# Kernel tuning notes

Hardware: AMD Instinct MI355X
Metric: run time of the kernel (lower is better)

The kernel has to match this reference:

```python
import jax, jax.numpy as jnp
import numpy as np

N = 65536      # total voxels (lidar + image tokens)
D = 256        # d_model
H = 8          # nhead
DFF = 2048     # dim_feedforward
SS = 128       # set_size
SN = 512       # set_num (SN * SS == N, each partition is a permutation of all voxels)
NSHIFT = 2


def setup_inputs() -> dict:
    key = jax.random.key(0)
    ks = jax.random.split(key, 10)
    src = jax.random.normal(ks[0], (N, D), jnp.float32)
    pos_embed = jax.random.normal(ks[1], (NSHIFT, N, D), jnp.float32) * 0.02
    # each (shift, set_id) partition covers every voxel exactly once
    inds = jnp.stack([
        jnp.stack([
            jax.random.permutation(jax.random.fold_in(ks[2], s * 2 + p), N).reshape(SN, SS)
            for p in range(2)
        ])
        for s in range(NSHIFT)
    ]).astype(jnp.int32)                      # (NSHIFT, 2, SN, SS)
    masks = jax.random.uniform(ks[3], (NSHIFT, 2, SN, SS)) < 0.1
    masks = masks.at[..., 0].set(False)       # keep at least one key per set
    init = lambda k, shape: jax.random.normal(k, shape, jnp.float32) * 0.02
    return {
        'src': src, 'pos_embed': pos_embed,
        'set_voxel_inds': inds, 'set_voxel_masks': masks,
        'w_qkv': init(ks[4], (2, 3 * D, D)), 'b_qkv': jnp.zeros((2, 3 * D)),
        'w_out': init(ks[5], (2, D, D)), 'b_out': jnp.zeros((2, D)),
        'w_ff1': init(ks[6], (2, DFF, D)), 'b_ff1': jnp.zeros((2, DFF)),
        'w_ff2': init(ks[7], (2, D, DFF)), 'b_ff2': jnp.zeros((2, D)),
        'g_n1': jnp.ones((2, D)), 'b_n1': jnp.zeros((2, D)),
        'g_n2': jnp.ones((2, D)), 'b_n2': jnp.zeros((2, D)),
        'g_ln': jnp.ones((2, D)), 'b_ln': jnp.zeros((2, D)),
    }


def _ln(x, g, b):
    m = jnp.mean(x, -1, keepdims=True)
    v = jnp.mean(jnp.square(x - m), -1, keepdims=True)
    return (x - m) * jax.lax.rsqrt(v + 1e-5) * g + b


def _mha(q_in, k_in, v_in, mask, wqkv, bqkv, wo, bo):
    # q_in/k_in/v_in: (SN, SS, D); mask: (SN, SS) True = ignore key
    wq, wk, wv = jnp.split(wqkv, 3, axis=0)
    bq, bk, bv = jnp.split(bqkv, 3, axis=0)
    hd = D // H
    q = (q_in @ wq.T + bq).reshape(SN, SS, H, hd)
    k = (k_in @ wk.T + bk).reshape(SN, SS, H, hd)
    v = (v_in @ wv.T + bv).reshape(SN, SS, H, hd)
    scores = jnp.einsum('bqhd,bkhd->bhqk', q, k) / np.float32(np.sqrt(hd))
    scores = jnp.where(mask[:, None, None, :], jnp.float32(-1e9), scores)
    attn = jax.nn.softmax(scores, axis=-1)
    o = jnp.einsum('bhqk,bkhd->bqhd', attn, v).reshape(SN, SS, D)
    return o @ wo.T + bo


def reference(src, pos_embed, set_voxel_inds, set_voxel_masks,
              w_qkv, b_qkv, w_out, b_out, w_ff1, b_ff1, w_ff2, b_ff2,
              g_n1, b_n1, g_n2, b_n2, g_ln, b_ln):
    out = src
    set_id = 0  # block_id % 2 with block_id == 0
    for i in range(NSHIFT):  # two encoder layers, one per shift
        inds = set_voxel_inds[i, set_id]   # (SN, SS)
        mask = set_voxel_masks[i, set_id]  # (SN, SS)
        pos = pos_embed[i]
        identity = out
        feat = out[inds]                   # gather voxels into sets
        qk = feat + pos[inds]
        a = _mha(qk, qk, feat, mask, w_qkv[i], b_qkv[i], w_out[i], b_out[i])
        # scatter back: per voxel, take its FIRST occurrence in flattened set order
        flat = inds.reshape(-1)
        L = flat.shape[0]
        perm = jnp.full((N,), L, jnp.int32).at[flat].min(jnp.arange(L, dtype=jnp.int32))
        src2 = a.reshape(-1, D)[perm]
        x = _ln(out + src2, g_n1[i], b_n1[i])
        ff = jax.nn.relu(x @ w_ff1[i].T + b_ff1[i]) @ w_ff2[i].T + b_ff2[i]
        x = _ln(x + ff, g_n2[i], b_n2[i])
        out = _ln(x + identity, g_ln[i], b_ln[i])
    return out
```

## Files before the change

kernel.cpp:

```cpp
#include <hip/hip_runtime.h>
#include <math.h>

#define NVOX 65536
#define DM 256
#define NH 8
#define HDIM 32
#define DFFN 2048
#define SSZ 128
#define SNUM 512

#define AS1 __attribute__((address_space(1)))
#define AS3 __attribute__((address_space(3)))

typedef __attribute__((ext_vector_type(8))) __bf16 bf16x8;
typedef __attribute__((ext_vector_type(8))) unsigned short u16x8;
typedef __attribute__((ext_vector_type(4))) float f32x4;

__device__ __forceinline__ unsigned short f2bf(float f) {
    unsigned int u = __float_as_uint(f);
    u += 0x7fffu + ((u >> 16) & 1u);
    return (unsigned short)(u >> 16);
}
__device__ __forceinline__ float bf2f(unsigned short u) {
    return __uint_as_float(((unsigned int)u) << 16);
}

#define VMCNT0 asm volatile("s_waitcnt vmcnt(0)" ::: "memory")
#define VMCNT2 asm volatile("s_waitcnt vmcnt(2)" ::: "memory")
#define VMCNT4 asm volatile("s_waitcnt vmcnt(4)" ::: "memory")
#define LGKM0  asm volatile("s_waitcnt lgkmcnt(0)" ::: "memory")

__global__ __launch_bounds__(256)
void cvt_bf16_kernel(const float* __restrict__ in, unsigned short* __restrict__ out, int n) {
    int i = blockIdx.x * 256 + threadIdx.x;
    int stride = gridDim.x * 256;
    for (; i < n; i += stride) out[i] = f2bf(in[i]);
}

__global__ __launch_bounds__(256)
void gather_kernel(const float* __restrict__ src, const float* __restrict__ pos,
                   const int* __restrict__ inds,
                   unsigned short* __restrict__ qk, unsigned short* __restrict__ feat) {
    int j = blockIdx.x * 4 + (threadIdx.x >> 6);
    int lane = threadIdx.x & 63;
    int v = inds[j];
    float4 a = ((const float4*)(src + (size_t)v * DM))[lane];
    float4 p = ((const float4*)(pos + (size_t)v * DM))[lane];
    ushort4 qo, fo;
    qo.x = f2bf(a.x + p.x); qo.y = f2bf(a.y + p.y);
    qo.z = f2bf(a.z + p.z); qo.w = f2bf(a.w + p.w);
    fo.x = f2bf(a.x); fo.y = f2bf(a.y); fo.z = f2bf(a.z); fo.w = f2bf(a.w);
    ((ushort4*)(qk   + (size_t)j * DM))[lane] = qo;
    ((ushort4*)(feat + (size_t)j * DM))[lane] = fo;
}

template<int EPI, bool RELU>
__global__ __launch_bounds__(512)
void gemm_mfma256(const unsigned short* __restrict__ A, const unsigned short* __restrict__ W,
                  const float* __restrict__ bias, void* __restrict__ Cout,
                  int M, int N, int K,
                  const int* __restrict__ inds,
                  const float* __restrict__ res1,
                  const float* __restrict__ g1, const float* __restrict__ b1,
                  unsigned short* __restrict__ out2) {
    __shared__ alignas(16) char smem[69632];
    unsigned short* As = (unsigned short*)smem;
    unsigned short* Bs = (unsigned short*)(smem + 32768);
    float* ebuf = (float*)smem;
    const int ES = 264;

    int tid = threadIdx.x;
    int wave = tid >> 6, lane = tid & 63;
    int wm = wave >> 2;
    int wn = wave & 3;

    unsigned lin = blockIdx.x + blockIdx.y * gridDim.x;
    unsigned nwg = gridDim.x * gridDim.y;
    unsigned swz = lin;
    if ((nwg & 7u) == 0u) { unsigned cpx = nwg >> 3; swz = (lin & 7u) * cpx + (lin >> 3); }
    int bx = (int)(swz / gridDim.y);
    int by = (int)(swz % gridDim.y);
    int mBase = bx * 256, nBase = by * 256;

    int rr = lane & 15;
    int kq = (lane >> 4) * 8;
    int rbase = (lane >> 4) * 4;

    f32x4 acc[8][4];
    const f32x4 zero = {0.f, 0.f, 0.f, 0.f};
#pragma unroll
    for (int m = 0; m < 8; m++)
#pragma unroll
        for (int n = 0; n < 4; n++) acc[m][n] = zero;

    const unsigned short* gA0 = A + (size_t)(mBase + (wave * 2 + 0) * 16 + rr) * K + kq;
    const unsigned short* gA1 = A + (size_t)(mBase + (wave * 2 + 1) * 16 + rr) * K + kq;
    const unsigned short* gB0 = W + (size_t)(nBase + (wave * 2 + 0) * 16 + rr) * K + kq;
    const unsigned short* gB1 = W + (size_t)(nBase + (wave * 2 + 1) * 16 + rr) * K + kq;

    auto stage = [&](int b, int kt) {
        int ko = kt * 32;
        __builtin_amdgcn_global_load_lds((const AS1 void*)(gA0 + ko),
            (AS3 void*)(As + b * 8192 + (wave * 2 + 0) * 512), 16, 0, 0);
        __builtin_amdgcn_global_load_lds((const AS1 void*)(gA1 + ko),
            (AS3 void*)(As + b * 8192 + (wave * 2 + 1) * 512), 16, 0, 0);
        __builtin_amdgcn_global_load_lds((const AS1 void*)(gB0 + ko),
            (AS3 void*)(Bs + b * 8192 + (wave * 2 + 0) * 512), 16, 0, 0);
        __builtin_amdgcn_global_load_lds((const AS1 void*)(gB1 + ko),
            (AS3 void*)(Bs + b * 8192 + (wave * 2 + 1) * 512), 16, 0, 0);
    };

    int nt = K >> 5;
    stage(0, 0);

    for (int t = 0; t < nt; ++t) {
        int p = t & 1;
        if (t + 1 < nt) { stage(p ^ 1, t + 1); VMCNT4; }
        else { VMCNT0; }
        __builtin_amdgcn_s_barrier();
        __builtin_amdgcn_sched_barrier(0);

        bf16x8 af[8], bf[4];
#pragma unroll
        for (int m = 0; m < 8; m++)
            af[m] = *(const bf16x8*)(As + p * 8192 + (wm * 8 + m) * 512 + lane * 8);
#pragma unroll
        for (int n = 0; n < 4; n++)
            bf[n] = *(const bf16x8*)(Bs + p * 8192 + (wn * 4 + n) * 512 + lane * 8);
#pragma unroll
        for (int m = 0; m < 8; m++)
#pragma unroll
            for (int n = 0; n < 4; n++)
                acc[m][n] = __builtin_amdgcn_mfma_f32_16x16x32_bf16(af[m], bf[n], acc[m][n], 0, 0, 0);

        __builtin_amdgcn_sched_barrier(0);
        __builtin_amdgcn_s_barrier();
    }

    float bn[4];
#pragma unroll
    for (int n = 0; n < 4; n++)
        bn[n] = bias[nBase + wn * 64 + n * 16 + rr];

    int erow = tid >> 3;
    int ec0  = (tid & 7) * 32;
#pragma unroll
    for (int pass = 0; pass < 4; ++pass) {
        __syncthreads();
        if (wm == (pass >> 1)) {
#pragma unroll
            for (int mm = 0; mm < 4; ++mm) {
                int m = (pass & 1) * 4 + mm;
#pragma unroll
                for (int n = 0; n < 4; ++n) {
                    int lcol = wn * 64 + n * 16 + rr;
#pragma unroll
                    for (int r = 0; r < 4; ++r) {
                        float v = acc[m][n][r] + bn[n];
                        if (RELU) v = fmaxf(v, 0.f);
                        ebuf[(mm * 16 + rbase + r) * ES + lcol] = v;
                    }
                }
            }
        }
        __syncthreads();
        int grow = mBase + pass * 64 + erow;

        if constexpr (EPI == 0) {
            unsigned short* dst = (unsigned short*)Cout + (size_t)grow * N + nBase + ec0;
#pragma unroll
            for (int g = 0; g < 4; ++g) {
                u16x8 o;
#pragma unroll
                for (int j = 0; j < 8; ++j)
                    o[j] = f2bf(ebuf[erow * ES + ec0 + g * 8 + j]);
                *(u16x8*)(dst + g * 8) = o;
            }
        } else {
            int v = inds[grow];
            const float* pr = res1 + (size_t)v * 256;
            f32x4 tv[8];
            float s = 0.f, s2 = 0.f;
#pragma unroll
            for (int g = 0; g < 8; ++g) {
                float4 e = *(float4*)(ebuf + erow * ES + ec0 + g * 4);
                float4 p = *(const float4*)(pr + ec0 + g * 4);
                f32x4 t = {e.x + p.x, e.y + p.y, e.z + p.z, e.w + p.w};
                tv[g] = t;
                s += t[0] + t[1] + t[2] + t[3];
                s2 += t[0]*t[0] + t[1]*t[1] + t[2]*t[2] + t[3]*t[3];
            }
#pragma unroll
            for (int off = 1; off < 8; off <<= 1) { s += __shfl_xor(s, off); s2 += __shfl_xor(s2, off); }
            float mean = s * (1.f/256.f);
            float var = fmaf(-mean, mean, s2 * (1.f/256.f));
            float rs = rsqrtf(var + 1e-5f);
            float* xd = (float*)Cout + (size_t)v * 256 + ec0;
            unsigned short* xb = out2 + (size_t)v * 256 + ec0;
#pragma unroll
            for (int g = 0; g < 8; ++g) {
                float4 gg = *(const float4*)(g1 + ec0 + g * 4);
                float4 bb = *(const float4*)(b1 + ec0 + g * 4);
                float4 o;
                o.x = fmaf((tv[g][0] - mean) * rs, gg.x, bb.x);
                o.y = fmaf((tv[g][1] - mean) * rs, gg.y, bb.y);
                o.z = fmaf((tv[g][2] - mean) * rs, gg.z, bb.z);
                o.w = fmaf((tv[g][3] - mean) * rs, gg.w, bb.w);
                *(float4*)(xd + g * 4) = o;
                ushort4 ob; ob.x = f2bf(o.x); ob.y = f2bf(o.y); ob.z = f2bf(o.z); ob.w = f2bf(o.w);
                *(ushort4*)(xb + g * 4) = ob;
            }
        }
    }
}

__global__ __launch_bounds__(512, 2)
void ffn_fused(const unsigned short* __restrict__ X,
               const unsigned short* __restrict__ W1,
               const unsigned short* __restrict__ W2,
               const float* __restrict__ b1g,
               const float* __restrict__ b2g,
               const float* __restrict__ xf,
               const float* __restrict__ prev,
               const float* __restrict__ lnG1, const float* __restrict__ lnB1,
               const float* __restrict__ lnG2, const float* __restrict__ lnB2,
               float* __restrict__ out) {
    __shared__ alignas(16) char smem[163840];
    unsigned short* Xs   = (unsigned short*)smem;
    unsigned short* Wbuf = (unsigned short*)(smem + 65536);
    char*           HsB  = smem + 98304;
    float*          ebuf = (float*)smem;
    const int ES = 264;

    int tid = threadIdx.x;
    int wave = tid >> 6, lane = tid & 63;
    int wm = wave >> 2;
    int wn = wave & 3;
    int mBase = blockIdx.x * 128;
    int rr = lane & 15;
    int kq = (lane >> 4) * 8;
    int rbase = (lane >> 4) * 4;

    auto gll = [&](const unsigned short* g, unsigned short* l) {
        __builtin_amdgcn_global_load_lds((const AS1 void*)g, (AS3 void*)l, 16, 0, 0);
    };

#pragma unroll
    for (int u = 0; u < 8; ++u)
        gll(X + (size_t)(mBase + wave * 16 + rr) * 256 + u * 32 + kq,
            Xs + (wave * 8 + u) * 512);

    auto stage_slice = [&](int s) {
        int c = s >> 4, half = (s >> 3) & 1, kt = s & 7;
        unsigned short* wb = Wbuf + (s & 1) * 8192;
        if (half == 0) {
            gll(W1 + (size_t)(c * 256 + (wave * 2 + 0) * 16 + rr) * 256 + kt * 32 + kq,
                wb + (wave * 2 + 0) * 512);
            gll(W1 + (size_t)(c * 256 + (wave * 2 + 1) * 16 + rr) * 256 + kt * 32 + kq,
                wb + (wave * 2 + 1) * 512);
        } else {
            gll(W2 + (size_t)((wave * 2 + 0) * 16 + rr) * 2048 + c * 256 + kt * 32 + kq,
                wb + (wave * 2 + 0) * 512);
            gll(W2 + (size_t)((wave * 2 + 1) * 16 + rr) * 2048 + c * 256 + kt * 32 + kq,
                wb + (wave * 2 + 1) * 512);
        }
    };

    f32x4 yacc[4][4];
    const f32x4 zero = {0.f, 0.f, 0.f, 0.f};
#pragma unroll
    for (int m = 0; m < 4; m++)
#pragma unroll
        for (int n = 0; n < 4; n++) yacc[m][n] = zero;

    stage_slice(0);
    __syncthreads();

    for (int c = 0; c < 8; ++c) {
        f32x4 hacc[4][4];
#pragma unroll
        for (int m = 0; m < 4; m++)
#pragma unroll
            for (int n = 0; n < 4; n++) hacc[m][n] = zero;

#pragma unroll
        for (int kt = 0; kt < 8; ++kt) {
            int s = c * 16 + kt;
            stage_slice(s + 1);
            VMCNT2;
            __builtin_amdgcn_s_barrier();
            __builtin_amdgcn_sched_barrier(0);

            bf16x8 af[4], bf[4];
#pragma unroll
            for (int m = 0; m < 4; m++)
                af[m] = *(const bf16x8*)(Xs + ((wm * 4 + m) * 8 + kt) * 512 + lane * 8);
#pragma unroll
            for (int n = 0; n < 4; n++)
                bf[n] = *(const bf16x8*)(Wbuf + (s & 1) * 8192 + (wn * 4 + n) * 512 + lane * 8);
#pragma unroll
            for (int m = 0; m < 4; m++)
#pragma unroll
                for (int n = 0; n < 4; n++)
                    hacc[m][n] = __builtin_amdgcn_mfma_f32_16x16x32_bf16(af[m], bf[n], hacc[m][n], 0, 0, 0);

            __builtin_amdgcn_sched_barrier(0);
            __builtin_amdgcn_s_barrier();
        }

        {
            float b1v[4];
#pragma unroll
            for (int n = 0; n < 4; n++)
                b1v[n] = b1g[c * 256 + wn * 64 + n * 16 + rr];
#pragma unroll
            for (int m = 0; m < 4; m++)
#pragma unroll
                for (int n = 0; n < 4; n++)
#pragma unroll
                    for (int r = 0; r < 4; r++) {
                        float v = fmaxf(hacc[m][n][r] + b1v[n], 0.f);
                        int row = wm * 64 + m * 16 + rbase + r;
                        int col = wn * 64 + n * 16 + rr;
                        unsigned byte = (unsigned)(row * 512 + col * 2) ^ ((row & 7) << 4);
                        *(unsigned short*)(HsB + byte) = f2bf(v);
                    }
            LGKM0;
            __builtin_amdgcn_s_barrier();
        }

#pragma unroll
        for (int kt = 0; kt < 8; ++kt) {
            int s = c * 16 + 8 + kt;
            if (s + 1 < 128) { stage_slice(s + 1); VMCNT2; }
            else { VMCNT0; }
            __builtin_amdgcn_s_barrier();
            __builtin_amdgcn_sched_barrier(0);

            bf16x8 af[4], bf[4];
#pragma unroll
            for (int m = 0; m < 4; m++) {
                int row = wm * 64 + m * 16 + rr;
                unsigned byte = (unsigned)(row * 512 + kt * 64 + (lane >> 4) * 16) ^ ((rr & 7) << 4);
                af[m] = *(const bf16x8*)(HsB + byte);
            }
#pragma unroll
            for (int n = 0; n < 4; n++)
                bf[n] = *(const bf16x8*)(Wbuf + (s & 1) * 8192 + (wn * 4 + n) * 512 + lane * 8);
#pragma unroll
            for (int m = 0; m < 4; m++)
#pragma unroll
                for (int n = 0; n < 4; n++)
                    yacc[m][n] = __builtin_amdgcn_mfma_f32_16x16x32_bf16(af[m], bf[n], yacc[m][n], 0, 0, 0);

            __builtin_amdgcn_sched_barrier(0);
            __builtin_amdgcn_s_barrier();
        }
    }

    float b2v[4];
#pragma unroll
    for (int n = 0; n < 4; n++)
        b2v[n] = b2g[wn * 64 + n * 16 + rr];

    int erow = tid >> 5;
    int ec0  = (tid & 31) * 8;
#pragma unroll
    for (int p = 0; p < 8; ++p) {
        __syncthreads();
        if (wm == (p >> 2)) {
            const int m = p & 3;
#pragma unroll
            for (int n = 0; n < 4; ++n) {
                int lcol = wn * 64 + n * 16 + rr;
#pragma unroll
                for (int r = 0; r < 4; ++r)
                    ebuf[(rbase + r) * ES + lcol] = yacc[m][n][r] + b2v[n];
            }
        }
        __syncthreads();
        int grow = mBase + p * 16 + erow;

        float tv[8];
        float s1 = 0.f, s2 = 0.f;
        const float* xr = xf + (size_t)grow * 256 + ec0;
#pragma unroll
        for (int j = 0; j < 8; ++j) {
            float t = ebuf[erow * ES + ec0 + j] + xr[j];
            tv[j] = t; s1 += t; s2 += t * t;
        }
#pragma unroll
        for (int off = 1; off < 32; off <<= 1) { s1 += __shfl_xor(s1, off); s2 += __shfl_xor(s2, off); }
        float mean = s1 * (1.f/256.f);
        float var = fmaf(-mean, mean, s2 * (1.f/256.f));
        float rs = rsqrtf(var + 1e-5f);

        const float* pr = prev + (size_t)grow * 256 + ec0;
        float s3 = 0.f, s4 = 0.f;
#pragma unroll
        for (int j = 0; j < 8; ++j) {
            float u = fmaf((tv[j] - mean) * rs, lnG1[ec0 + j], lnB1[ec0 + j]) + pr[j];
            tv[j] = u; s3 += u; s4 += u * u;
        }
#pragma unroll
        for (int off = 1; off < 32; off <<= 1) { s3 += __shfl_xor(s3, off); s4 += __shfl_xor(s4, off); }
        float mean2 = s3 * (1.f/256.f);
        float var2 = fmaf(-mean2, mean2, s4 * (1.f/256.f));
        float rs2 = rsqrtf(var2 + 1e-5f);

        float* od = out + (size_t)grow * 256 + ec0;
#pragma unroll
        for (int g = 0; g < 2; ++g) {
            float4 o;
            o.x = fmaf((tv[g*4+0] - mean2) * rs2, lnG2[ec0 + g*4+0], lnB2[ec0 + g*4+0]);
            o.y = fmaf((tv[g*4+1] - mean2) * rs2, lnG2[ec0 + g*4+1], lnB2[ec0 + g*4+1]);
            o.z = fmaf((tv[g*4+2] - mean2) * rs2, lnG2[ec0 + g*4+2], lnB2[ec0 + g*4+2]);
            o.w = fmaf((tv[g*4+3] - mean2) * rs2, lnG2[ec0 + g*4+3], lnB2[ec0 + g*4+3]);
            *(float4*)(od + g * 4) = o;
        }
    }
}

__global__ __launch_bounds__(256)
void attn_mfma_kernel(const unsigned short* __restrict__ QK,
                      const unsigned short* __restrict__ V,
                      const unsigned char* __restrict__ mask,
                      unsigned short* __restrict__ ao) {
    int s = blockIdx.x, h = blockIdx.y;
    int tid = threadIdx.x;
    int wq = tid >> 6;
    int lane = tid & 63;

    __shared__ alignas(16) unsigned short Ks[128 * 40];
    __shared__ alignas(16) unsigned short Vt[32 * 136];
    __shared__ alignas(16) unsigned short Plds[4 * 4096];
    __shared__ unsigned char msk[SSZ];

#pragma unroll
    for (int it = 0; it < 2; it++) {
        int idx = tid + it * 256;
        int key = idx >> 2, dimoff = (idx & 3) * 8;
        bf16x8 kv = *(const bf16x8*)(QK + (size_t)(s * SSZ + key) * 512 + 256 + h * HDIM + dimoff);
        *(bf16x8*)(Ks + key * 40 + dimoff) = kv;
        u16x8 vv = *(const u16x8*)(V + (size_t)(s * SSZ + key) * DM + h * HDIM + dimoff);
#pragma unroll
        for (int j = 0; j < 8; j++) Vt[(dimoff + j) * 136 + key] = vv[j];
    }
    if (tid < SSZ) msk[tid] = mask[s * SSZ + tid];
    __syncthreads();

    int rr = lane & 15;
    int kq = (lane >> 4) * 8;
    const f32x4 zero = {0.f, 0.f, 0.f, 0.f};

    bf16x8 qa[2];
#pragma unroll
    for (int mt = 0; mt < 2; mt++)
        qa[mt] = *(const bf16x8*)(QK + (size_t)(s * SSZ + wq * 32 + mt * 16 + rr) * 512 + h * HDIM + kq);

    f32x4 S[2][8];
#pragma unroll
    for (int nt = 0; nt < 8; nt++) {
        bf16x8 kb = *(const bf16x8*)(Ks + (nt * 16 + rr) * 40 + kq);
#pragma unroll
        for (int mt = 0; mt < 2; mt++)
            S[mt][nt] = __builtin_amdgcn_mfma_f32_16x16x32_bf16(qa[mt], kb, zero, 0, 0, 0);
    }

    const float SCALE = 0.17677669529663687f;
    f32x4 rm[2];
#pragma unroll
    for (int mt = 0; mt < 2; mt++) { rm[mt].x = rm[mt].y = rm[mt].z = rm[mt].w = -1e30f; }
#pragma unroll
    for (int nt = 0; nt < 8; nt++) {
        bool mv = msk[nt * 16 + rr] != 0;
#pragma unroll
        for (int mt = 0; mt < 2; mt++) {
#pragma unroll
            for (int r = 0; r < 4; r++) {
                float v = mv ? -1e30f : S[mt][nt][r] * SCALE;
                S[mt][nt][r] = v;
                rm[mt][r] = fmaxf(rm[mt][r], v);
            }
        }
    }
#pragma unroll
    for (int off = 1; off < 16; off <<= 1) {
#pragma unroll
        for (int mt = 0; mt < 2; mt++)
#pragma unroll
            for (int r = 0; r < 4; r++)
                rm[mt][r] = fmaxf(rm[mt][r], __shfl_xor(rm[mt][r], off));
    }

    f32x4 rs[2];
#pragma unroll
    for (int mt = 0; mt < 2; mt++) { rs[mt] = zero; }
#pragma unroll
    for (int nt = 0; nt < 8; nt++)
#pragma unroll
        for (int mt = 0; mt < 2; mt++)
#pragma unroll
            for (int r = 0; r < 4; r++) {
                float p = __expf(S[mt][nt][r] - rm[mt][r]);
                S[mt][nt][r] = p;
                rs[mt][r] += p;
            }
#pragma unroll
    for (int off = 1; off < 16; off <<= 1) {
#pragma unroll
        for (int mt = 0; mt < 2; mt++)
#pragma unroll
            for (int r = 0; r < 4; r++)
                rs[mt][r] += __shfl_xor(rs[mt][r], off);
    }

    char* Pbase = (char*)Plds + wq * 8192;
#pragma unroll
    for (int nt = 0; nt < 8; nt++)
#pragma unroll
        for (int mt = 0; mt < 2; mt++)
#pragma unroll
            for (int r = 0; r < 4; r++) {
                int prow = mt * 16 + (lane >> 4) * 4 + r;
                int col  = nt * 16 + rr;
                unsigned addr = (unsigned)(prow * 256 + col * 2) ^ ((prow & 7) << 4);
                *(unsigned short*)(Pbase + addr) = f2bf(S[mt][nt][r]);
            }
    __syncthreads();

    f32x4 O[2][2];
#pragma unroll
    for (int mt = 0; mt < 2; mt++)
#pragma unroll
        for (int nd = 0; nd < 2; nd++) O[mt][nd] = zero;
#pragma unroll
    for (int kc = 0; kc < 4; kc++) {
        bf16x8 pa[2];
#pragma unroll
        for (int mt = 0; mt < 2; mt++) {
            int prow = mt * 16 + rr;
            unsigned addr = (unsigned)(prow * 256 + (kc * 32 + kq) * 2) ^ ((prow & 7) << 4);
            pa[mt] = *(const bf16x8*)(Pbase + addr);
        }
#pragma unroll
        for (int nd = 0; nd < 2; nd++) {
            bf16x8 vb = *(const bf16x8*)(Vt + (nd * 16 + rr) * 136 + kc * 32 + kq);
#pragma unroll
            for (int mt = 0; mt < 2; mt++)
                O[mt][nd] = __builtin_amdgcn_mfma_f32_16x16x32_bf16(pa[mt], vb, O[mt][nd], 0, 0, 0);
        }
    }

#pragma unroll
    for (int mt = 0; mt < 2; mt++) {
#pragma unroll
        for (int nd = 0; nd < 2; nd++) {
#pragma unroll
            for (int r = 0; r < 4; r++) {
                int row = s * SSZ + wq * 32 + mt * 16 + (lane >> 4) * 4 + r;
                int col = h * HDIM + nd * 16 + rr;
                ao[(size_t)row * DM + col] = f2bf(O[mt][nd][r] / rs[mt][r]);
            }
        }
    }
}

extern "C" void kernel_launch(void* const* d_in, const int* in_sizes, int n_in,
                              void* d_out, int out_size, void* d_ws, size_t ws_size,
                              hipStream_t stream) {
    const float* src       = (const float*)d_in[0];
    const float* pos_embed = (const float*)d_in[1];
    const int*   inds_all  = (const int*)d_in[2];
    const unsigned char* masks_all = (const unsigned char*)d_in[3];
    const float* w_qkv = (const float*)d_in[4];
    const float* b_qkv = (const float*)d_in[5];
    const float* w_out = (const float*)d_in[6];
    const float* b_out = (const float*)d_in[7];
    const float* w_ff1 = (const float*)d_in[8];
    const float* b_ff1 = (const float*)d_in[9];
    const float* w_ff2 = (const float*)d_in[10];
    const float* b_ff2 = (const float*)d_in[11];
    const float* g_n1 = (const float*)d_in[12];
    const float* b_n1 = (const float*)d_in[13];
    const float* g_n2 = (const float*)d_in[14];
    const float* b_n2 = (const float*)d_in[15];
    const float* g_ln = (const float*)d_in[16];
    const float* b_ln = (const float*)d_in[17];
    float* out = (float*)d_out;

    const size_t NVF = (size_t)NVOX * DM;
    unsigned short* A = (unsigned short*)d_ws;
    unsigned short* B = A + NVF;
    unsigned short* C = B + NVF;
    unsigned short* D = C + 2 * NVF;
    float* F = (float*)(D + NVF);
    unsigned short* wts = (unsigned short*)(F + NVF);
    const size_t SZ_QKV = (size_t)2 * 3 * DM * DM;
    const size_t SZ_WO  = (size_t)2 * DM * DM;
    const size_t SZ_FF1 = (size_t)2 * DFFN * DM;
    const size_t SZ_FF2 = (size_t)2 * DM * DFFN;
    unsigned short* wqkv_bf = wts;
    unsigned short* wo_bf   = wqkv_bf + SZ_QKV;
    unsigned short* wff1_bf = wo_bf + SZ_WO;
    unsigned short* wff2_bf = wff1_bf + SZ_FF1;

    cvt_bf16_kernel<<<512, 256, 0, stream>>>(w_qkv, wqkv_bf, (int)SZ_QKV);
    cvt_bf16_kernel<<<256, 256, 0, stream>>>(w_out, wo_bf, (int)SZ_WO);
    cvt_bf16_kernel<<<1024, 256, 0, stream>>>(w_ff1, wff1_bf, (int)SZ_FF1);
    cvt_bf16_kernel<<<1024, 256, 0, stream>>>(w_ff2, wff2_bf, (int)SZ_FF2);

    for (int i = 0; i < 2; i++) {
        const float* prev = (i == 0) ? src : out;
        const int* inds = inds_all + (size_t)i * 2 * SNUM * SSZ;
        const unsigned char* mask = masks_all + (size_t)i * 2 * SNUM * SSZ;
        const float* pos  = pos_embed + (size_t)i * NVF;
        const unsigned short* wqkv = wqkv_bf + (size_t)i * 3 * DM * DM;
        const unsigned short* wo   = wo_bf + (size_t)i * DM * DM;
        const unsigned short* wff1 = wff1_bf + (size_t)i * DFFN * DM;
        const unsigned short* wff2 = wff2_bf + (size_t)i * DM * DFFN;
        const float* bqkv = b_qkv + (size_t)i * 3 * DM;
        const float* bo   = b_out + (size_t)i * DM;
        const float* bff1 = b_ff1 + (size_t)i * DFFN;
        const float* bff2 = b_ff2 + (size_t)i * DM;

        gather_kernel<<<NVOX / 4, 256, 0, stream>>>(prev, pos, inds, A, B);

        gemm_mfma256<0, false><<<dim3(NVOX / 256, 512 / 256), 512, 0, stream>>>(
            A, wqkv, bqkv, C, NVOX, 512, DM,
            nullptr, nullptr, nullptr, nullptr, nullptr);
        gemm_mfma256<0, false><<<dim3(NVOX / 256, 1), 512, 0, stream>>>(
            B, wqkv + (size_t)512 * DM, bqkv + 512, D, NVOX, DM, DM,
            nullptr, nullptr, nullptr, nullptr, nullptr);

        attn_mfma_kernel<<<dim3(SNUM, NH), 256, 0, stream>>>(C, D, mask, A);

        gemm_mfma256<2, false><<<dim3(NVOX / 256, 1), 512, 0, stream>>>(
            A, wo, bo, F, NVOX, DM, DM,
            inds, prev, g_n1 + i * DM, b_n1 + i * DM, B);

        ffn_fused<<<dim3(NVOX / 128), 512, 0, stream>>>(
            B, wff1, wff2, bff1, bff2, F, prev,
            g_n2 + i * DM, b_n2 + i * DM, g_ln + i * DM, b_ln + i * DM, out);
    }
}
```

Baseline: 1.023 ms.

## Load FFN weight fragments directly into registers instead of staging through LDS

The fused FFN kernel no longer stages W1/W2 slices into a double-buffered LDS region with per-step barriers. Each wave now loads its own B fragments from global memory straight into registers, one k-step ahead, and the per-k-step barriers are removed. This also frees 32 KB of shared memory. In exchange, each weight row is loaded separately by both wm wave groups with no LDS sharing, which doubles global/L2 traffic, and prefetch latency hiding now depends on the compiler's scheduling.

```diff
diff --git a/kernel.cpp b/kernel.cpp
--- a/kernel.cpp
+++ b/kernel.cpp
@@ -26,9 +26,7 @@
 }
 
 #define VMCNT0 asm volatile("s_waitcnt vmcnt(0)" ::: "memory")
-#define VMCNT2 asm volatile("s_waitcnt vmcnt(2)" ::: "memory")
 #define VMCNT4 asm volatile("s_waitcnt vmcnt(4)" ::: "memory")
-#define LGKM0  asm volatile("s_waitcnt lgkmcnt(0)" ::: "memory")
 
 __global__ __launch_bounds__(256)
 void cvt_bf16_kernel(const float* __restrict__ in, unsigned short* __restrict__ out, int n) {
@@ -225,10 +223,9 @@
                const float* __restrict__ lnG1, const float* __restrict__ lnB1,
                const float* __restrict__ lnG2, const float* __restrict__ lnB2,
                float* __restrict__ out) {
-    __shared__ alignas(16) char smem[163840];
-    unsigned short* Xs   = (unsigned short*)smem;
-    unsigned short* Wbuf = (unsigned short*)(smem + 65536);
-    char*           HsB  = smem + 98304;
+    __shared__ alignas(16) char smem[131072];
+    unsigned short* Xs = (unsigned short*)smem;
+    char*           HsB = smem + 65536;
     float*          ebuf = (float*)smem;
     const int ES = 264;
 
@@ -241,29 +238,21 @@
     int kq = (lane >> 4) * 8;
     int rbase = (lane >> 4) * 4;
 
-    auto gll = [&](const unsigned short* g, unsigned short* l) {
-        __builtin_amdgcn_global_load_lds((const AS1 void*)g, (AS3 void*)l, 16, 0, 0);
+#pragma unroll
+    for (int u = 0; u < 8; ++u)
+        __builtin_amdgcn_global_load_lds(
+            (const AS1 void*)(X + (size_t)(mBase + wave * 16 + rr) * 256 + u * 32 + kq),
+            (AS3 void*)(Xs + (wave * 8 + u) * 512), 16, 0, 0);
+
+    auto loadW1 = [&](int c, int kt, bf16x8* dst) {
+#pragma unroll
+        for (int n = 0; n < 4; n++)
+            dst[n] = *(const bf16x8*)(W1 + (size_t)(c * 256 + wn * 64 + n * 16 + rr) * 256 + kt * 32 + kq);
     };
-
-#pragma unroll
-    for (int u = 0; u < 8; ++u)
-        gll(X + (size_t)(mBase + wave * 16 + rr) * 256 + u * 32 + kq,
-            Xs + (wave * 8 + u) * 512);
-
-    auto stage_slice = [&](int s) {
-        int c = s >> 4, half = (s >> 3) & 1, kt = s & 7;
-        unsigned short* wb = Wbuf + (s & 1) * 8192;
-        if (half == 0) {
-            gll(W1 + (size_t)(c * 256 + (wave * 2 + 0) * 16 + rr) * 256 + kt * 32 + kq,
-                wb + (wave * 2 + 0) * 512);
-            gll(W1 + (size_t)(c * 256 + (wave * 2 + 1) * 16 + rr) * 256 + kt * 32 + kq,
-                wb + (wave * 2 + 1) * 512);
-        } else {
-            gll(W2 + (size_t)((wave * 2 + 0) * 16 + rr) * 2048 + c * 256 + kt * 32 + kq,
-                wb + (wave * 2 + 0) * 512);
-            gll(W2 + (size_t)((wave * 2 + 1) * 16 + rr) * 2048 + c * 256 + kt * 32 + kq,
-                wb + (wave * 2 + 1) * 512);
-        }
+    auto loadW2 = [&](int c, int kt, bf16x8* dst) {
+#pragma unroll
+        for (int n = 0; n < 4; n++)
+            dst[n] = *(const bf16x8*)(W2 + (size_t)(wn * 64 + n * 16 + rr) * 2048 + c * 256 + kt * 32 + kq);
     };
 
     f32x4 yacc[4][4];
@@ -273,7 +262,8 @@
 #pragma unroll
         for (int n = 0; n < 4; n++) yacc[m][n] = zero;
 
-    stage_slice(0);
+    bf16x8 bfc[4], bfn[4];
+    loadW1(0, 0, bfc);
     __syncthreads();
 
     for (int c = 0; c < 8; ++c) {
@@ -285,29 +275,22 @@
 
 #pragma unroll
         for (int kt = 0; kt < 8; ++kt) {
-            int s = c * 16 + kt;
-            stage_slice(s + 1);
-            VMCNT2;
-            __builtin_amdgcn_s_barrier();
-            __builtin_amdgcn_sched_barrier(0);
-
-            bf16x8 af[4], bf[4];
+            if (kt < 7) loadW1(c, kt + 1, bfn);
+            else        loadW2(c, 0, bfn);
+            bf16x8 af[4];
 #pragma unroll
             for (int m = 0; m < 4; m++)
                 af[m] = *(const bf16x8*)(Xs + ((wm * 4 + m) * 8 + kt) * 512 + lane * 8);
 #pragma unroll
-            for (int n = 0; n < 4; n++)
-                bf[n] = *(const bf16x8*)(Wbuf + (s & 1) * 8192 + (wn * 4 + n) * 512 + lane * 8);
-#pragma unroll
             for (int m = 0; m < 4; m++)
 #pragma unroll
                 for (int n = 0; n < 4; n++)
-                    hacc[m][n] = __builtin_amdgcn_mfma_f32_16x16x32_bf16(af[m], bf[n], hacc[m][n], 0, 0, 0);
-
-            __builtin_amdgcn_sched_barrier(0);
-            __builtin_amdgcn_s_barrier();
-        }
-
+                    hacc[m][n] = __builtin_amdgcn_mfma_f32_16x16x32_bf16(af[m], bfc[n], hacc[m][n], 0, 0, 0);
+#pragma unroll
+            for (int n = 0; n < 4; n++) bfc[n] = bfn[n];
+        }
+
+        __syncthreads();
         {
             float b1v[4];
 #pragma unroll
@@ -325,19 +308,14 @@
                         unsigned byte = (unsigned)(row * 512 + col * 2) ^ ((row & 7) << 4);
                         *(unsigned short*)(HsB + byte) = f2bf(v);
                     }
-            LGKM0;
-            __builtin_amdgcn_s_barrier();
-        }
+        }
+        __syncthreads();
 
 #pragma unroll
         for (int kt = 0; kt < 8; ++kt) {
-            int s = c * 16 + 8 + kt;
-            if (s + 1 < 128) { stage_slice(s + 1); VMCNT2; }
-            else { VMCNT0; }
-            __builtin_amdgcn_s_barrier();
-            __builtin_amdgcn_sched_barrier(0);
-
-            bf16x8 af[4], bf[4];
+            if (kt < 7)      loadW2(c, kt + 1, bfn);
+            else if (c < 7)  loadW1(c + 1, 0, bfn);
+            bf16x8 af[4];
 #pragma unroll
             for (int m = 0; m < 4; m++) {
                 int row = wm * 64 + m * 16 + rr;
@@ -345,16 +323,12 @@
                 af[m] = *(const bf16x8*)(HsB + byte);
             }
 #pragma unroll
-            for (int n = 0; n < 4; n++)
-                bf[n] = *(const bf16x8*)(Wbuf + (s & 1) * 8192 + (wn * 4 + n) * 512 + lane * 8);
-#pragma unroll
             for (int m = 0; m < 4; m++)
 #pragma unroll
                 for (int n = 0; n < 4; n++)
-                    yacc[m][n] = __builtin_amdgcn_mfma_f32_16x16x32_bf16(af[m], bf[n], yacc[m][n], 0, 0, 0);
-
-            __builtin_amdgcn_sched_barrier(0);
-            __builtin_amdgcn_s_barrier();
+                    yacc[m][n] = __builtin_amdgcn_mfma_f32_16x16x32_bf16(af[m], bfc[n], yacc[m][n], 0, 0, 0);
+#pragma unroll
+            for (int n = 0; n < 4; n++) bfc[n] = bfn[n];
         }
     }
 
```

Result: slower. 1.183 ms (+15.6%).

## Run fused FFN kernel with 16 waves per block instead of 8

Applied to the files above, without the earlier changes.

Doubles the ffn_fused block from 512 to 1024 threads. Each wave now owns a 64x32 output sub-tile instead of 64x64, and each thread issues one weight-slice load per stage instead of two. The X-tile load, the waitcnt thresholds and the LayerNorm epilogue (64 lanes per row, 4 columns each) are remapped to match. The aim is more waves per block to hide latency and lower per-wave register pressure, at the cost of smaller MFMA tiles with less register reuse of A fragments, more barrier participants and one extra __syncthreads per chunk.

```diff
diff --git a/kernel.cpp b/kernel.cpp
--- a/kernel.cpp
+++ b/kernel.cpp
@@ -26,7 +26,7 @@
 }
 
 #define VMCNT0 asm volatile("s_waitcnt vmcnt(0)" ::: "memory")
-#define VMCNT2 asm volatile("s_waitcnt vmcnt(2)" ::: "memory")
+#define VMCNT1 asm volatile("s_waitcnt vmcnt(1)" ::: "memory")
 #define VMCNT4 asm volatile("s_waitcnt vmcnt(4)" ::: "memory")
 #define LGKM0  asm volatile("s_waitcnt lgkmcnt(0)" ::: "memory")
 
@@ -214,7 +214,7 @@
     }
 }
 
-__global__ __launch_bounds__(512, 2)
+__global__ __launch_bounds__(1024, 1)
 void ffn_fused(const unsigned short* __restrict__ X,
                const unsigned short* __restrict__ W1,
                const unsigned short* __restrict__ W2,
@@ -234,8 +234,8 @@
 
     int tid = threadIdx.x;
     int wave = tid >> 6, lane = tid & 63;
-    int wm = wave >> 2;
-    int wn = wave & 3;
+    int wm = wave >> 3;
+    int wn = wave & 7;
     int mBase = blockIdx.x * 128;
     int rr = lane & 15;
     int kq = (lane >> 4) * 8;
@@ -246,82 +246,81 @@
     };
 
 #pragma unroll
-    for (int u = 0; u < 8; ++u)
-        gll(X + (size_t)(mBase + wave * 16 + rr) * 256 + u * 32 + kq,
-            Xs + (wave * 8 + u) * 512);
+    for (int u = 0; u < 4; ++u) {
+        int st = wave * 4 + u;
+        gll(X + (size_t)(mBase + (st >> 3) * 16 + rr) * 256 + (st & 7) * 32 + kq,
+            Xs + st * 512);
+    }
 
     auto stage_slice = [&](int s) {
         int c = s >> 4, half = (s >> 3) & 1, kt = s & 7;
         unsigned short* wb = Wbuf + (s & 1) * 8192;
         if (half == 0) {
-            gll(W1 + (size_t)(c * 256 + (wave * 2 + 0) * 16 + rr) * 256 + kt * 32 + kq,
-                wb + (wave * 2 + 0) * 512);
-            gll(W1 + (size_t)(c * 256 + (wave * 2 + 1) * 16 + rr) * 256 + kt * 32 + kq,
-                wb + (wave * 2 + 1) * 512);
+            gll(W1 + (size_t)(c * 256 + wave * 16 + rr) * 256 + kt * 32 + kq,
+                wb + wave * 512);
         } else {
-            gll(W2 + (size_t)((wave * 2 + 0) * 16 + rr) * 2048 + c * 256 + kt * 32 + kq,
-                wb + (wave * 2 + 0) * 512);
-            gll(W2 + (size_t)((wave * 2 + 1) * 16 + rr) * 2048 + c * 256 + kt * 32 + kq,
-                wb + (wave * 2 + 1) * 512);
+            gll(W2 + (size_t)(wave * 16 + rr) * 2048 + c * 256 + kt * 32 + kq,
+                wb + wave * 512);
         }
     };
 
-    f32x4 yacc[4][4];
+    f32x4 yacc[4][2];
     const f32x4 zero = {0.f, 0.f, 0.f, 0.f};
 #pragma unroll
     for (int m = 0; m < 4; m++)
 #pragma unroll
-        for (int n = 0; n < 4; n++) yacc[m][n] = zero;
+        for (int n = 0; n < 2; n++) yacc[m][n] = zero;
 
     stage_slice(0);
     __syncthreads();
 
     for (int c = 0; c < 8; ++c) {
-        f32x4 hacc[4][4];
+        f32x4 hacc[4][2];
 #pragma unroll
         for (int m = 0; m < 4; m++)
 #pragma unroll
-            for (int n = 0; n < 4; n++) hacc[m][n] = zero;
+            for (int n = 0; n < 2; n++) hacc[m][n] = zero;
 
 #pragma unroll
         for (int kt = 0; kt < 8; ++kt) {
             int s = c * 16 + kt;
             stage_slice(s + 1);
-            VMCNT2;
+            VMCNT1;
             __builtin_amdgcn_s_barrier();
             __builtin_amdgcn_sched_barrier(0);
 
-            bf16x8 af[4], bf[4];
+            bf16x8 af[4], bf[2];
 #pragma unroll
             for (int m = 0; m < 4; m++)
                 af[m] = *(const bf16x8*)(Xs + ((wm * 4 + m) * 8 + kt) * 512 + lane * 8);
 #pragma unroll
-            for (int n = 0; n < 4; n++)
-                bf[n] = *(const bf16x8*)(Wbuf + (s & 1) * 8192 + (wn * 4 + n) * 512 + lane * 8);
+            for (int n = 0; n < 2; n++)
+                bf[n] = *(const bf16x8*)(Wbuf + (s & 1) * 8192 + (wn * 2 + n) * 512 + lane * 8);
 #pragma unroll
             for (int m = 0; m < 4; m++)
 #pragma unroll
-                for (int n = 0; n < 4; n++)
+                for (int n = 0; n < 2; n++)
                     hacc[m][n] = __builtin_amdgcn_mfma_f32_16x16x32_bf16(af[m], bf[n], hacc[m][n], 0, 0, 0);
 
             __builtin_amdgcn_sched_barrier(0);
             __builtin_amdgcn_s_barrier();
         }
 
+        __syncthreads();
         {
-            float b1v[4];
-#pragma unroll
-            for (int n = 0; n < 4; n++)
-                b1v[n] = b1g[c * 256 + wn * 64 + n * 16 + rr];
+            float b1v[2];
+#pragma unroll
+            for (int n = 0; n < 2; n++)
+                b1v[n] = b1g[c * 256 + wn * 32 + n * 16 + rr];
 #pragma unroll
             for (int m = 0; m < 4; m++)
 #pragma unroll
-                for (int n = 0; n < 4; n++)
+                for (int n = 0; n < 2; n++)
 #pragma unroll
                     for (int r = 0; r < 4; r++) {
                         float v = fmaxf(hacc[m][n][r] + b1v[n], 0.f);
                         int row = wm * 64 + m * 16 + rbase + r;
-                        int col = wn * 64 + n * 16 + rr;
+                        int col = wn * 32 + n * 16 + rr;
                         unsigned byte = (unsigned)(row * 512 + col * 2) ^ ((row & 7) << 4);
                         *(unsigned short*)(HsB + byte) = f2bf(v);
                     }
@@ -332,12 +331,12 @@
 #pragma unroll
         for (int kt = 0; kt < 8; ++kt) {
             int s = c * 16 + 8 + kt;
-            if (s + 1 < 128) { stage_slice(s + 1); VMCNT2; }
+            if (s + 1 < 128) { stage_slice(s + 1); VMCNT1; }
             else { VMCNT0; }
             __builtin_amdgcn_s_barrier();
             __builtin_amdgcn_sched_barrier(0);
 
-            bf16x8 af[4], bf[4];
+            bf16x8 af[4], bf[2];
 #pragma unroll
             for (int m = 0; m < 4; m++) {
                 int row = wm * 64 + m * 16 + rr;
@@ -345,12 +344,12 @@
                 af[m] = *(const bf16x8*)(HsB + byte);
             }
 #pragma unroll
-            for (int n = 0; n < 4; n++)
-                bf[n] = *(const bf16x8*)(Wbuf + (s & 1) * 8192 + (wn * 4 + n) * 512 + lane * 8);
+            for (int n = 0; n < 2; n++)
+                bf[n] = *(const bf16x8*)(Wbuf + (s & 1) * 8192 + (wn * 2 + n) * 512 + lane * 8);
 #pragma unroll
             for (int m = 0; m < 4; m++)
 #pragma unroll
-                for (int n = 0; n < 4; n++)
+                for (int n = 0; n < 2; n++)
                     yacc[m][n] = __builtin_amdgcn_mfma_f32_16x16x32_bf16(af[m], bf[n], yacc[m][n], 0, 0, 0);
 
             __builtin_amdgcn_sched_barrier(0);
@@ -358,21 +357,21 @@
         }
     }
 
-    float b2v[4];
-#pragma unroll
-    for (int n = 0; n < 4; n++)
-        b2v[n] = b2g[wn * 64 + n * 16 + rr];
-
-    int erow = tid >> 5;
-    int ec0  = (tid & 31) * 8;
+    float b2v[2];
+#pragma unroll
+    for (int n = 0; n < 2; n++)
+        b2v[n] = b2g[wn * 32 + n * 16 + rr];
+
+    int erow = tid >> 6;
+    int ec0  = (tid & 63) * 4;
 #pragma unroll
     for (int p = 0; p < 8; ++p) {
         __syncthreads();
         if (wm == (p >> 2)) {
             const int m = p & 3;
 #pragma unroll
-            for (int n = 0; n < 4; ++n) {
-                int lcol = wn * 64 + n * 16 + rr;
+            for (int n = 0; n < 2; ++n) {
+                int lcol = wn * 32 + n * 16 + rr;
 #pragma unroll
                 for (int r = 0; r < 4; ++r)
                     ebuf[(rbase + r) * ES + lcol] = yacc[m][n][r] + b2v[n];
@@ -381,16 +380,16 @@
         __syncthreads();
         int grow = mBase + p * 16 + erow;
 
-        float tv[8];
+        float tv[4];
         float s1 = 0.f, s2 = 0.f;
         const float* xr = xf + (size_t)grow * 256 + ec0;
 #pragma unroll
-        for (int j = 0; j < 8; ++j) {
+        for (int j = 0; j < 4; ++j) {
             float t = ebuf[erow * ES + ec0 + j] + xr[j];
             tv[j] = t; s1 += t; s2 += t * t;
         }
 #pragma unroll
-        for (int off = 1; off < 32; off <<= 1) { s1 += __shfl_xor(s1, off); s2 += __shfl_xor(s2, off); }
+        for (int off = 1; off < 64; off <<= 1) { s1 += __shfl_xor(s1, off); s2 += __shfl_xor(s2, off); }
         float mean = s1 * (1.f/256.f);
         float var = fmaf(-mean, mean, s2 * (1.f/256.f));
         float rs = rsqrtf(var + 1e-5f);
@@ -398,26 +397,23 @@
         const float* pr = prev + (size_t)grow * 256 + ec0;
         float s3 = 0.f, s4 = 0.f;
 #pragma unroll
-        for (int j = 0; j < 8; ++j) {
+        for (int j = 0; j < 4; ++j) {
             float u = fmaf((tv[j] - mean) * rs, lnG1[ec0 + j], lnB1[ec0 + j]) + pr[j];
             tv[j] = u; s3 += u; s4 += u * u;
         }
 #pragma unroll
-        for (int off = 1; off < 32; off <<= 1) { s3 += __shfl_xor(s3, off); s4 += __shfl_xor(s4, off); }
+        for (int off = 1; off < 64; off <<= 1) { s3 += __shfl_xor(s3, off); s4 += __shfl_xor(s4, off); }
         float mean2 = s3 * (1.f/256.f);
         float var2 = fmaf(-mean2, mean2, s4 * (1.f/256.f));
         float rs2 = rsqrtf(var2 + 1e-5f);
 
         float* od = out + (size_t)grow * 256 + ec0;
-#pragma unroll
-        for (int g = 0; g < 2; ++g) {
-            float4 o;
-            o.x = fmaf((tv[g*4+0] - mean2) * rs2, lnG2[ec0 + g*4+0], lnB2[ec0 + g*4+0]);
-            o.y = fmaf((tv[g*4+1] - mean2) * rs2, lnG2[ec0 + g*4+1], lnB2[ec0 + g*4+1]);
-            o.z = fmaf((tv[g*4+2] - mean2) * rs2, lnG2[ec0 + g*4+2], lnB2[ec0 + g*4+2]);
-            o.w = fmaf((tv[g*4+3] - mean2) * rs2, lnG2[ec0 + g*4+3], lnB2[ec0 + g*4+3]);
-            *(float4*)(od + g * 4) = o;
-        }
+        float4 o;
+        o.x = fmaf((tv[0] - mean2) * rs2, lnG2[ec0 + 0], lnB2[ec0 + 0]);
+        o.y = fmaf((tv[1] - mean2) * rs2, lnG2[ec0 + 1], lnB2[ec0 + 1]);
+        o.z = fmaf((tv[2] - mean2) * rs2, lnG2[ec0 + 2], lnB2[ec0 + 2]);
+        o.w = fmaf((tv[3] - mean2) * rs2, lnG2[ec0 + 3], lnB2[ec0 + 3]);
+        *(float4*)od = o;
     }
 }
 
@@ -639,7 +635,7 @@
             A, wo, bo, F, NVOX, DM, DM,
             inds, prev, g_n1 + i * DM, b_n1 + i * DM, B);
 
-        ffn_fused<<<dim3(NVOX / 128), 512, 0, stream>>>(
+        ffn_fused<<<dim3(NVOX / 128), 1024, 0, stream>>>(
             B, wff1, wff2, bff1, bff2, F, prev,
             g_n2 + i * DM, b_n2 + i * DM, g_ln + i * DM, b_ln + i * DM, out);
     }
```

Result: slower. 1.317 ms (+28.7%).
